# Performance work log

Hardware: AMD Instinct MI355X
Metric: run time of the kernel (lower is better)

## Reference

```python
import jax, jax.numpy as jnp
import numpy as np

MAX_FREQ = 4
OMEGA = 0.5 * np.pi
PATCH = 64


def _unnorm(c, size):
    # align_corners=False convention of torch.grid_sample
    return ((c + 1.0) * size - 1.0) / 2.0


def _gather(im, yy, xx):
    # im [C,H,W], yy/xx [Ho,Wo] -> [C,Ho,Wo]
    return im[:, yy, xx]


def _gs_nearest(inp, grid):
    # inp [B,C,H,W], grid [B,Ho,Wo,2] (x,y); padding_mode='border'
    B, C, H, W = inp.shape
    x = jnp.clip(jnp.round(_unnorm(grid[..., 0], W)), 0, W - 1).astype(jnp.int32)
    y = jnp.clip(jnp.round(_unnorm(grid[..., 1], H)), 0, H - 1).astype(jnp.int32)
    return jax.vmap(_gather)(inp, y, x)  # [B,C,Ho,Wo]


def _gs_bilinear(inp, grid):
    B, C, H, W = inp.shape
    x = jnp.clip(_unnorm(grid[..., 0], W), 0.0, W - 1.0)
    y = jnp.clip(_unnorm(grid[..., 1], H), 0.0, H - 1.0)
    x0 = jnp.floor(x); y0 = jnp.floor(y)
    wx = (x - x0)[:, None]; wy = (y - y0)[:, None]  # [B,1,Ho,Wo]
    x0i = x0.astype(jnp.int32); y0i = y0.astype(jnp.int32)
    x1i = jnp.minimum(x0i + 1, W - 1); y1i = jnp.minimum(y0i + 1, H - 1)
    g = jax.vmap(_gather)
    v00 = g(inp, y0i, x0i); v01 = g(inp, y0i, x1i)
    v10 = g(inp, y1i, x0i); v11 = g(inp, y1i, x1i)
    return (v00 * (1 - wx) * (1 - wy) + v01 * wx * (1 - wy)
            + v10 * (1 - wx) * wy + v11 * wx * wy)


def _conv2d(x, w, b):
    y = jax.lax.conv_general_dilated(x, w, (1, 1), ((1, 1), (1, 1)),
                                     dimension_numbers=("NCHW", "OIHW", "NCHW"))
    return y + b[None, :, None, None]


def _lc_decoder(q, rel):
    # q [B,Ho,Wo,2F+1], rel [B,Ho,Wo,1]; Fourier basis [1, cos(k*w*rel), sin(k*w*rel)]
    k = jnp.arange(1, MAX_FREQ + 1, dtype=q.dtype)
    ang = rel * k * OMEGA  # [B,Ho,Wo,F]
    basis = jnp.concatenate([jnp.ones_like(rel), jnp.cos(ang), jnp.sin(ang)], axis=-1)
    return jnp.sum(q * basis, axis=-1, keepdims=True)  # [B,Ho,Wo,1]


def _forward(sinogram, feat, grid, square_inv, adapt_w, adapt_b):
    B = feat.shape[0]
    sino = _conv2d(feat, adapt_w, adapt_b)          # [B,2F+1,V,D]
    V, D = sino.shape[-2], sino.shape[-1]
    # make_coord along detector axis (dim=1 coord channel), padding=0
    coord_d = ((jnp.arange(D, dtype=sino.dtype) + 0.5) / D) * 2.0 - 1.0
    sino_coord = jnp.broadcast_to(coord_d[None, None, None, :], (B, 1, V, D))
    shift_interval = 1.0 / D
    eps = 1e-4
    q_recons, lengths = [], []
    for sx in (-shift_interval, shift_interval):  # ensembling shifts
        g = grid + jnp.array([sx, 0.0], dtype=grid.dtype) + 1e-6
        q_recon = jnp.transpose(_gs_nearest(sino, g), (0, 2, 3, 1))       # [B,V,P2,2F+1]
        q_coord = jnp.transpose(_gs_nearest(sino_coord, g), (0, 2, 3, 1))  # [B,V,P2,1]
        rel = (grid[..., 0:1] - q_coord) * D
        q_recons.append(_lc_decoder(q_recon, rel))
        lengths.append(jnp.abs(rel) + eps)
    tot = lengths[0] + lengths[1]
    # lengths are swapped before weighting (cross weighting)
    recon = q_recons[0] * lengths[1] / tot + q_recons[1] * lengths[0] / tot
    out = jnp.sum(jnp.transpose(recon, (0, 3, 1, 2)) * square_inv * 10000.0, axis=-2)
    # back projection of center channel of raw sinogram
    ch = sinogram.shape[1]
    bp = _gs_bilinear(sinogram[:, ch // 2:ch // 2 + 1], grid)
    out = out + jnp.sum(bp * square_inv * 10000.0, axis=-2)  # [B,1,P2]
    return out.reshape(B, 1, PATCH, PATCH)


def setup_inputs() -> dict:
    key = jax.random.key(0)
    ks = jax.random.split(key, 6)
    B, V, D, ENC = 4, 360, 512, 64
    P2 = PATCH * PATCH
    CH = 2 * MAX_FREQ + 1
    return {
        "sinogram": jax.random.normal(ks[0], (B, 1, V, D), jnp.float32),
        "feat": jax.random.normal(ks[1], (B, ENC, V, D), jnp.float32),
        "grid": jax.random.uniform(ks[2], (B, V, P2, 2), jnp.float32, -1.0, 1.0),
        "square_inv": jax.random.uniform(ks[3], (B, 1, V, P2), jnp.float32, 1e-5, 1e-4),
        "adapt_w": jax.random.normal(ks[4], (CH, ENC, 3, 3), jnp.float32) * 0.05,
        "adapt_b": jax.random.normal(ks[5], (CH,), jnp.float32) * 0.05,
    }


def reference(sinogram, feat, grid, square_inv, adapt_w, adapt_b):
    return _forward(sinogram, feat, grid, square_inv, adapt_w, adapt_b)
```

## Files before the change

### kernel.cpp

```cpp
#include <hip/hip_runtime.h>
#include <hip/hip_fp16.h>
#include <math.h>

#define B   4
#define V   360
#define D   512
#define ENC 64
#define CH  9
#define P2  4096
#define NCHUNK 90
#define VCHUNK 4
#define DPT 4
#define RECH 16

__global__ __launch_bounds__(256) void conv_kernel(
    const float* __restrict__ feat,
    const float* __restrict__ w,
    const float* __restrict__ bias,
    __half* __restrict__ sino)
{
    const int bid = blockIdx.x;
    const int sw  = (bid & 7) * 90 + (bid >> 3);
    const int b   = sw / 180;
    const int vt  = sw % 180;
    const int tr  = threadIdx.x >> 7;
    const int v   = vt * 2 + tr;
    const int d0  = (threadIdx.x & 127) * DPT;

    float acc[CH][DPT];
    #pragma unroll
    for (int oc = 0; oc < CH; ++oc) {
        const float bv = bias[oc];
        #pragma unroll
        for (int p = 0; p < DPT; ++p) acc[oc][p] = bv;
    }

    const float* fb = feat + ((size_t)b * ENC * V + v) * D + d0;
    const bool vm = v > 0, vp = v < V - 1;
    const bool dm = d0 > 0, dp = (d0 + DPT) < D;

    for (int ic = 0; ic < ENC; ++ic) {
        const float* f = fb + (size_t)ic * (V * D);
        float r[3][DPT + 2];
        #pragma unroll
        for (int rr = 0; rr < 3; ++rr) {
            const float* fr = f + (rr - 1) * D;
            const bool ok = (rr == 0) ? vm : ((rr == 2) ? vp : true);
            float4 c = ok ? *(const float4*)fr : float4{0.f, 0.f, 0.f, 0.f};
            r[rr][1] = c.x; r[rr][2] = c.y; r[rr][3] = c.z; r[rr][4] = c.w;
            r[rr][0] = (ok && dm) ? fr[-1]  : 0.f;
            r[rr][5] = (ok && dp) ? fr[DPT] : 0.f;
        }
        #pragma unroll
        for (int oc = 0; oc < CH; ++oc) {
            const float* ww = w + ((size_t)oc * ENC + ic) * 9;
            #pragma unroll
            for (int kr = 0; kr < 3; ++kr) {
                #pragma unroll
                for (int kc = 0; kc < 3; ++kc) {
                    const float wv = ww[kr * 3 + kc];
                    #pragma unroll
                    for (int p = 0; p < DPT; ++p)
                        acc[oc][p] = fmaf(r[kr][p + kc], wv, acc[oc][p]);
                }
            }
        }
    }

    #pragma unroll
    for (int p = 0; p < DPT; ++p) {
        __half* rec = sino + (size_t)(((size_t)b * V + v) * D + d0 + p) * RECH;
        union { __half2 h; unsigned u; } cv;
        uint4 pk;
        cv.h = __floats2half2_rn(acc[0][p], acc[1][p]); pk.x = cv.u;
        cv.h = __floats2half2_rn(acc[2][p], acc[3][p]); pk.y = cv.u;
        cv.h = __floats2half2_rn(acc[4][p], acc[5][p]); pk.z = cv.u;
        cv.h = __floats2half2_rn(acc[6][p], acc[7][p]); pk.w = cv.u;
        *(uint4*)rec = pk;
        cv.h = __floats2half2_rn(acc[8][p], 0.f);
        *(unsigned*)(rec + 8) = cv.u;
    }
}

__global__ __launch_bounds__(256) void build_sg2(
    const float* __restrict__ sg, float2* __restrict__ sg2)
{
    const int i = blockIdx.x * 256 + threadIdx.x;
    const int x = i & (D - 1);
    const float a = sg[i];
    const float c = (x == D - 1) ? a : sg[i + 1];
    sg2[i] = float2{a, c};
}

template <int PAIRED>
__global__ __launch_bounds__(256) void sample_kernel(
    const __half* __restrict__ sino,
    const float* __restrict__ sinogram,
    const float2* __restrict__ sg2,
    const float* __restrict__ grid,
    const float* __restrict__ sq,
    float* __restrict__ partial)
{
    const int bid = blockIdx.x;
    const int xcd = bid & 7;
    const int b   = xcd >> 1;
    const int idx = ((bid >> 3) << 1) | (xcd & 1);
    const int chunk = idx >> 4;
    const int p  = (idx & 15) * 256 + threadIdx.x;
    const int v0 = chunk * VCHUNK;

    const float*  sg  = sinogram + (size_t)b * V * D;
    const float2* sg2b = sg2 + (size_t)b * V * D;
    const __half* sb  = sino + (size_t)b * V * D * RECH;

    float gx[4], gy[4], sv[4];
    #pragma unroll
    for (int u = 0; u < 4; ++u) {
        const size_t gi = (size_t)(b * V + v0 + u) * P2 + p;
        const double gd = __builtin_nontemporal_load((const double*)grid + gi);
        const unsigned long long gu = __double_as_longlong(gd);
        gx[u] = __uint_as_float((unsigned)gu);
        gy[u] = __uint_as_float((unsigned)(gu >> 32));
        sv[u] = __builtin_nontemporal_load(sq + gi);
    }

    uint4    ra[4][2];
    unsigned rzu[4][2];
    float    rel[4][2];
    #pragma unroll
    for (int u = 0; u < 4; ++u) {
        const float fy = ((gy[u] + 1e-6f + 1.f) * (float)V - 1.f) * 0.5f;
        const int   yi = (int)fminf(fmaxf(rintf(fy), 0.f), (float)(V - 1));
        const float fx0 = ((gx[u] + 1e-6f + 1.f) * (float)D - 1.f) * 0.5f;
        #pragma unroll
        for (int sft = 0; sft < 2; ++sft) {
            const float fx = (sft == 0) ? (fx0 - 0.5f) : (fx0 + 0.5f);
            const int   xi = (int)fminf(fmaxf(rintf(fx), 0.f), (float)(D - 1));
            const float qc = ((float)xi + 0.5f) * (2.f / (float)D) - 1.f;
            rel[u][sft] = (gx[u] - qc) * (float)D;
            const __half* rec = sb + (size_t)(yi * D + xi) * RECH;
            ra[u][sft]  = *(const uint4*)rec;
            rzu[u][sft] = *(const unsigned*)(rec + 8);
        }
    }

    float bl00[4], bl01[4], bl10[4], bl11[4], wxv[4], wyv[4];
    #pragma unroll
    for (int u = 0; u < 4; ++u) {
        float fxb = fminf(fmaxf(((gx[u] + 1.f) * (float)D - 1.f) * 0.5f, 0.f), (float)(D - 1));
        float fyb = fminf(fmaxf(((gy[u] + 1.f) * (float)V - 1.f) * 0.5f, 0.f), (float)(V - 1));
        const float x0 = floorf(fxb), y0 = floorf(fyb);
        wxv[u] = fxb - x0; wyv[u] = fyb - y0;
        const int x0i = (int)x0, y0i = (int)y0;
        const int y1i = min(y0i + 1, V - 1);
        if (PAIRED) {
            const float2 t = sg2b[y0i * D + x0i];
            const float2 u2 = sg2b[y1i * D + x0i];
            bl00[u] = t.x;  bl01[u] = t.y;
            bl10[u] = u2.x; bl11[u] = u2.y;
        } else {
            const int x1i = min(x0i + 1, D - 1);
            bl00[u] = sg[y0i * D + x0i]; bl01[u] = sg[y0i * D + x1i];
            bl10[u] = sg[y1i * D + x0i]; bl11[u] = sg[y1i * D + x1i];
        }
    }

    float acc = 0.f;
    #pragma unroll
    for (int u = 0; u < 4; ++u) {
        float val[2], len[2];
        #pragma unroll
        for (int sft = 0; sft < 2; ++sft) {
            float q[9];
            {
                const uint4 a = ra[u][sft];
                union { unsigned uu; __half2 h; } c;
                float2 f;
                c.uu = a.x; f = __half22float2(c.h); q[0] = f.x; q[1] = f.y;
                c.uu = a.y; f = __half22float2(c.h); q[2] = f.x; q[3] = f.y;
                c.uu = a.z; f = __half22float2(c.h); q[4] = f.x; q[5] = f.y;
                c.uu = a.w; f = __half22float2(c.h); q[6] = f.x; q[7] = f.y;
                union { unsigned short us; __half hh; } c2;
                c2.us = (unsigned short)rzu[u][sft];
                q[8] = __half2float(c2.hh);
            }
            const float r = rel[u][sft];
            const float ang = r * 1.5707963267948966f;
            float s1, c1;
            __sincosf(ang, &s1, &c1);
            const float c2 = fmaf(2.f * c1, c1, -1.f);
            const float s2 = 2.f * c1 * s1;
            const float c3 = fmaf(2.f * c1, c2, -c1);
            const float s3 = fmaf(2.f * c1, s2, -s1);
            const float c4 = fmaf(2.f * c1, c3, -c2);
            const float s4 = fmaf(2.f * c1, s3, -s2);

            float vv = q[0];
            vv = fmaf(q[1], c1, vv); vv = fmaf(q[2], c2, vv);
            vv = fmaf(q[3], c3, vv); vv = fmaf(q[4], c4, vv);
            vv = fmaf(q[5], s1, vv); vv = fmaf(q[6], s2, vv);
            vv = fmaf(q[7], s3, vv); vv = fmaf(q[8], s4, vv);
            val[sft] = vv;
            len[sft] = fabsf(r) + 1e-4f;
        }
        const float tot   = len[0] + len[1];
        const float recon = (val[0] * len[1] + val[1] * len[0]) / tot;

        const float wx = wxv[u], wy = wyv[u];
        const float bp = bl00[u] * (1.f - wx) * (1.f - wy) + bl01[u] * wx * (1.f - wy)
                       + bl10[u] * (1.f - wx) * wy         + bl11[u] * wx * wy;

        acc += (recon + bp) * sv[u] * 1e4f;
    }
    __builtin_nontemporal_store(acc, partial + ((size_t)chunk * B + b) * P2 + p);
}

__global__ __launch_bounds__(256) void reduce_kernel(
    const float* __restrict__ partial, float* __restrict__ out)
{
    const int i = blockIdx.x * 256 + threadIdx.x;
    float a = 0.f;
    #pragma unroll 6
    for (int c = 0; c < NCHUNK; ++c)
        a += __builtin_nontemporal_load(partial + (size_t)c * B * P2 + i);
    out[i] = a;
}

extern "C" void kernel_launch(void* const* d_in, const int* in_sizes, int n_in,
                              void* d_out, int out_size, void* d_ws, size_t ws_size,
                              hipStream_t stream)
{
    const float* sinogram = (const float*)d_in[0];
    const float* feat     = (const float*)d_in[1];
    const float* grid     = (const float*)d_in[2];
    const float* sq       = (const float*)d_in[3];
    const float* w        = (const float*)d_in[4];
    const float* bias     = (const float*)d_in[5];
    float* out = (float*)d_out;

    const size_t sino_b = (size_t)B * V * D * RECH * sizeof(__half);
    const size_t part_b = (size_t)NCHUNK * B * P2 * sizeof(float);
    const size_t sg2_b  = (size_t)B * V * D * sizeof(float2);

    __half* sino    = (__half*)d_ws;
    float*  partial = (float*)((char*)d_ws + sino_b);
    float2* sg2     = (float2*)((char*)d_ws + sino_b + part_b);
    const bool paired = (ws_size >= sino_b + part_b + sg2_b);

    conv_kernel<<<dim3(720), 256, 0, stream>>>(feat, w, bias, sino);
    if (paired) {
        build_sg2<<<dim3(2880), 256, 0, stream>>>(sinogram, sg2);
        sample_kernel<1><<<dim3(5760), 256, 0, stream>>>(sino, sinogram, sg2, grid, sq, partial);
    } else {
        sample_kernel<0><<<dim3(5760), 256, 0, stream>>>(sino, sinogram, sg2, grid, sq, partial);
    }
    reduce_kernel<<<dim3((B * P2) / 256), 256, 0, stream>>>(partial, out);
}
```

Baseline: 278.3 us.

## Store conv records as adjacent-pair entries so each sample does one fetch

The conv output is rewritten into a padded per-row layout of 513 64-byte entries. Each entry holds the records for detector columns x-1 and x side by side, so the two nearest-neighbour records a sample point needs sit in the same cache line. The conv kernel now computes two outputs per thread over 1440 blocks, double-buffers its input rows across channels, and writes each record twice. The aim is fewer scattered cache-line misses in the sampling gather, paid for with a larger intermediate buffer and more write traffic from the conv.

```diff
diff --git a/kernel.cpp b/kernel.cpp
--- a/kernel.cpp
+++ b/kernel.cpp
@@ -10,47 +10,49 @@
 #define P2  4096
 #define NCHUNK 90
 #define VCHUNK 4
-#define DPT 4
 #define RECH 16
-
+#define PENT 513
+#define PENTB 64
+
+template <int PAIR>
 __global__ __launch_bounds__(256) void conv_kernel(
     const float* __restrict__ feat,
     const float* __restrict__ w,
     const float* __restrict__ bias,
-    __half* __restrict__ sino)
+    char* __restrict__ outp)
 {
     const int bid = blockIdx.x;
-    const int sw  = (bid & 7) * 90 + (bid >> 3);
-    const int b   = sw / 180;
-    const int vt  = sw % 180;
-    const int tr  = threadIdx.x >> 7;
-    const int v   = vt * 2 + tr;
-    const int d0  = (threadIdx.x & 127) * DPT;
-
-    float acc[CH][DPT];
+    const int sw  = (bid & 7) * 180 + (bid >> 3);
+    const int b   = sw / V;
+    const int v   = sw % V;
+    const int d0  = threadIdx.x * 2;
+
+    float acc[CH][2];
     #pragma unroll
     for (int oc = 0; oc < CH; ++oc) {
         const float bv = bias[oc];
-        #pragma unroll
-        for (int p = 0; p < DPT; ++p) acc[oc][p] = bv;
+        acc[oc][0] = bv; acc[oc][1] = bv;
     }
 
     const float* fb = feat + ((size_t)b * ENC * V + v) * D + d0;
     const bool vm = v > 0, vp = v < V - 1;
-    const bool dm = d0 > 0, dp = (d0 + DPT) < D;
-
-    for (int ic = 0; ic < ENC; ++ic) {
+    const bool dm = d0 > 0, dp = d0 + 2 < D;
+
+    float r0[3][4], r1[3][4];
+
+    auto ld = [&](float r[3][4], int ic) {
         const float* f = fb + (size_t)ic * (V * D);
-        float r[3][DPT + 2];
         #pragma unroll
         for (int rr = 0; rr < 3; ++rr) {
             const float* fr = f + (rr - 1) * D;
             const bool ok = (rr == 0) ? vm : ((rr == 2) ? vp : true);
-            float4 c = ok ? *(const float4*)fr : float4{0.f, 0.f, 0.f, 0.f};
-            r[rr][1] = c.x; r[rr][2] = c.y; r[rr][3] = c.z; r[rr][4] = c.w;
-            r[rr][0] = (ok && dm) ? fr[-1]  : 0.f;
-            r[rr][5] = (ok && dp) ? fr[DPT] : 0.f;
-        }
+            float2 c = ok ? *(const float2*)fr : float2{0.f, 0.f};
+            r[rr][1] = c.x; r[rr][2] = c.y;
+            r[rr][0] = (ok && dm) ? fr[-1] : 0.f;
+            r[rr][3] = (ok && dp) ? fr[2]  : 0.f;
+        }
+    };
+    auto fmab = [&](const float r[3][4], int ic) {
         #pragma unroll
         for (int oc = 0; oc < CH; ++oc) {
             const float* ww = w + ((size_t)oc * ENC + ic) * 9;
@@ -59,26 +61,55 @@
                 #pragma unroll
                 for (int kc = 0; kc < 3; ++kc) {
                     const float wv = ww[kr * 3 + kc];
-                    #pragma unroll
-                    for (int p = 0; p < DPT; ++p)
-                        acc[oc][p] = fmaf(r[kr][p + kc], wv, acc[oc][p]);
+                    acc[oc][0] = fmaf(r[kr][kc],     wv, acc[oc][0]);
+                    acc[oc][1] = fmaf(r[kr][kc + 1], wv, acc[oc][1]);
                 }
             }
         }
-    }
-
-    #pragma unroll
-    for (int p = 0; p < DPT; ++p) {
-        __half* rec = sino + (size_t)(((size_t)b * V + v) * D + d0 + p) * RECH;
+    };
+
+    ld(r0, 0);
+    #pragma unroll 1
+    for (int ic = 0; ic < ENC; ic += 2) {
+        ld(r1, ic + 1);
+        fmab(r0, ic);
+        if (ic + 2 < ENC) ld(r0, ic + 2);
+        fmab(r1, ic + 1);
+    }
+
+    #pragma unroll
+    for (int p = 0; p < 2; ++p) {
         union { __half2 h; unsigned u; } cv;
         uint4 pk;
         cv.h = __floats2half2_rn(acc[0][p], acc[1][p]); pk.x = cv.u;
         cv.h = __floats2half2_rn(acc[2][p], acc[3][p]); pk.y = cv.u;
         cv.h = __floats2half2_rn(acc[4][p], acc[5][p]); pk.z = cv.u;
         cv.h = __floats2half2_rn(acc[6][p], acc[7][p]); pk.w = cv.u;
-        *(uint4*)rec = pk;
         cv.h = __floats2half2_rn(acc[8][p], 0.f);
-        *(unsigned*)(rec + 8) = cv.u;
+        const unsigned short z = (unsigned short)(cv.u & 0xffffu);
+        const int x = d0 + p;
+        if (PAIR) {
+            char* row = outp + (size_t)(b * V + v) * PENT * PENTB;
+            char* eA = row + (size_t)(x + 1) * PENTB;
+            *(uint4*)eA = pk;
+            *(unsigned short*)(eA + 32) = z;
+            char* eB = row + (size_t)x * PENTB + 16;
+            *(uint4*)eB = pk;
+            *(unsigned short*)(eB + 18) = z;
+            if (x == 0) {
+                *(uint4*)row = pk;
+                *(unsigned short*)(row + 32) = z;
+            }
+            if (x == D - 1) {
+                char* eC = row + (size_t)512 * PENTB + 16;
+                *(uint4*)eC = pk;
+                *(unsigned short*)(eC + 18) = z;
+            }
+        } else {
+            __half* rec = (__half*)outp + (size_t)(((size_t)b * V + v) * D + x) * RECH;
+            *(uint4*)rec = pk;
+            *(unsigned*)(rec + 8) = (unsigned)z;
+        }
     }
 }
 
@@ -92,10 +123,39 @@
     sg2[i] = float2{a, c};
 }
 
-template <int PAIRED>
-__global__ __launch_bounds__(256) void sample_kernel(
-    const __half* __restrict__ sino,
-    const float* __restrict__ sinogram,
+__device__ __forceinline__ float decode_rec(uint4 a, unsigned short z, float rel)
+{
+    float q[9];
+    union { unsigned uu; __half2 h; } c;
+    float2 f;
+    c.uu = a.x; f = __half22float2(c.h); q[0] = f.x; q[1] = f.y;
+    c.uu = a.y; f = __half22float2(c.h); q[2] = f.x; q[3] = f.y;
+    c.uu = a.z; f = __half22float2(c.h); q[4] = f.x; q[5] = f.y;
+    c.uu = a.w; f = __half22float2(c.h); q[6] = f.x; q[7] = f.y;
+    union { unsigned short us; __half hh; } c2;
+    c2.us = z;
+    q[8] = __half2float(c2.hh);
+
+    const float ang = rel * 1.5707963267948966f;
+    float s1, c1;
+    __sincosf(ang, &s1, &c1);
+    const float c2f = fmaf(2.f * c1, c1, -1.f);
+    const float s2f = 2.f * c1 * s1;
+    const float c3f = fmaf(2.f * c1, c2f, -c1);
+    const float s3f = fmaf(2.f * c1, s2f, -s1);
+    const float c4f = fmaf(2.f * c1, c3f, -c2f);
+    const float s4f = fmaf(2.f * c1, s3f, -s2f);
+
+    float vv = q[0];
+    vv = fmaf(q[1], c1,  vv); vv = fmaf(q[2], c2f, vv);
+    vv = fmaf(q[3], c3f, vv); vv = fmaf(q[4], c4f, vv);
+    vv = fmaf(q[5], s1,  vv); vv = fmaf(q[6], s2f, vv);
+    vv = fmaf(q[7], s3f, vv); vv = fmaf(q[8], s4f, vv);
+    return vv;
+}
+
+__global__ __launch_bounds__(256) void sample_pair(
+    const char* __restrict__ pair,
     const float2* __restrict__ sg2,
     const float* __restrict__ grid,
     const float* __restrict__ sq,
@@ -109,9 +169,8 @@
     const int p  = (idx & 15) * 256 + threadIdx.x;
     const int v0 = chunk * VCHUNK;
 
-    const float*  sg  = sinogram + (size_t)b * V * D;
-    const float2* sg2b = sg2 + (size_t)b * V * D;
-    const __half* sb  = sino + (size_t)b * V * D * RECH;
+    const char*   pb  = pair + (size_t)b * V * PENT * PENTB;
+    const float2* s2b = sg2 + (size_t)b * V * D;
 
     float gx[4], gy[4], sv[4];
     #pragma unroll
@@ -124,8 +183,96 @@
         sv[u] = __builtin_nontemporal_load(sq + gi);
     }
 
+    uint4 qa[4], qb[4];
+    unsigned short zA[4], zB[4];
+    float relm[4], relp[4];
+    #pragma unroll
+    for (int u = 0; u < 4; ++u) {
+        const float fy = ((gy[u] + 1e-6f + 1.f) * (float)V - 1.f) * 0.5f;
+        const int   yi = (int)fminf(fmaxf(rintf(fy), 0.f), (float)(V - 1));
+        const float fx0 = ((gx[u] + 1e-6f + 1.f) * (float)D - 1.f) * 0.5f;
+        const int xm = (int)fminf(fmaxf(rintf(fx0 - 0.5f), 0.f), (float)(D - 1));
+        const int xp = (int)fminf(fmaxf(rintf(fx0 + 0.5f), 0.f), (float)(D - 1));
+        const float qcm = ((float)xm + 0.5f) * (2.f / (float)D) - 1.f;
+        const float qcp = ((float)xp + 0.5f) * (2.f / (float)D) - 1.f;
+        relm[u] = (gx[u] - qcm) * (float)D;
+        relp[u] = (gx[u] - qcp) * (float)D;
+        const char* rowp = pb + (size_t)yi * (PENT * PENTB);
+        const char* e1 = rowp + (size_t)(xm + 1) * PENTB;
+        const char* e2 = rowp + (size_t)xp * PENTB;
+        qa[u] = *(const uint4*)e1;
+        zA[u] = *(const unsigned short*)(e1 + 32);
+        qb[u] = *(const uint4*)(e2 + 16);
+        zB[u] = *(const unsigned short*)(e2 + 34);
+    }
+
+    float bl00[4], bl01[4], bl10[4], bl11[4], wxv[4], wyv[4];
+    #pragma unroll
+    for (int u = 0; u < 4; ++u) {
+        float fxb = fminf(fmaxf(((gx[u] + 1.f) * (float)D - 1.f) * 0.5f, 0.f), (float)(D - 1));
+        float fyb = fminf(fmaxf(((gy[u] + 1.f) * (float)V - 1.f) * 0.5f, 0.f), (float)(V - 1));
+        const float x0 = floorf(fxb), y0 = floorf(fyb);
+        wxv[u] = fxb - x0; wyv[u] = fyb - y0;
+        const int x0i = (int)x0, y0i = (int)y0;
+        const int y1i = min(y0i + 1, V - 1);
+        const float2 t  = s2b[y0i * D + x0i];
+        const float2 u2 = s2b[y1i * D + x0i];
+        bl00[u] = t.x;  bl01[u] = t.y;
+        bl10[u] = u2.x; bl11[u] = u2.y;
+    }
+
+    float acc = 0.f;
+    #pragma unroll
+    for (int u = 0; u < 4; ++u) {
+        const float vmv = decode_rec(qa[u], zA[u], relm[u]);
+        const float vpv = decode_rec(qb[u], zB[u], relp[u]);
+        const float lm = fabsf(relm[u]) + 1e-4f;
+        const float lp = fabsf(relp[u]) + 1e-4f;
+        const float recon = (vmv * lp + vpv * lm) / (lm + lp);
+
+        const float wx = wxv[u], wy = wyv[u];
+        const float bp = bl00[u] * (1.f - wx) * (1.f - wy) + bl01[u] * wx * (1.f - wy)
+                       + bl10[u] * (1.f - wx) * wy         + bl11[u] * wx * wy;
+
+        acc += (recon + bp) * sv[u] * 1e4f;
+    }
+    __builtin_nontemporal_store(acc, partial + ((size_t)chunk * B + b) * P2 + p);
+}
+
+template <int PAIRED>
+__global__ __launch_bounds__(256) void sample_basic(
+    const __half* __restrict__ sino,
+    const float* __restrict__ sinogram,
+    const float2* __restrict__ sg2,
+    const float* __restrict__ grid,
+    const float* __restrict__ sq,
+    float* __restrict__ partial)
+{
+    const int bid = blockIdx.x;
+    const int xcd = bid & 7;
+    const int b   = xcd >> 1;
+    const int idx = ((bid >> 3) << 1) | (xcd & 1);
+    const int chunk = idx >> 4;
+    const int p  = (idx & 15) * 256 + threadIdx.x;
+    const int v0 = chunk * VCHUNK;
+
+    const float*  sg   = sinogram + (size_t)b * V * D;
+    const float2* s2b  = sg2 + (size_t)b * V * D;
+    const __half* sb   = sino + (size_t)b * V * D * RECH;
+
+    float gx[4], gy[4], sv[4];
+    #pragma unroll
+    for (int u = 0; u < 4; ++u) {
+        const size_t gi = (size_t)(b * V + v0 + u) * P2 + p;
+        const double gd = __builtin_nontemporal_load((const double*)grid + gi);
+        const unsigned long long gu = __double_as_longlong(gd);
+        gx[u] = __uint_as_float((unsigned)gu);
+        gy[u] = __uint_as_float((unsigned)(gu >> 32));
+        sv[u] = __builtin_nontemporal_load(sq + gi);
+    }
+
     uint4    ra[4][2];
-    unsigned rzu[4][2];
+    unsigned rz[4][2];
     float    rel[4][2];
     #pragma unroll
     for (int u = 0; u < 4; ++u) {
@@ -139,8 +286,8 @@
             const float qc = ((float)xi + 0.5f) * (2.f / (float)D) - 1.f;
             rel[u][sft] = (gx[u] - qc) * (float)D;
             const __half* rec = sb + (size_t)(yi * D + xi) * RECH;
-            ra[u][sft]  = *(const uint4*)rec;
-            rzu[u][sft] = *(const unsigned*)(rec + 8);
+            ra[u][sft] = *(const uint4*)rec;
+            rz[u][sft] = *(const unsigned*)(rec + 8);
         }
     }
 
@@ -154,8 +301,8 @@
         const int x0i = (int)x0, y0i = (int)y0;
         const int y1i = min(y0i + 1, V - 1);
         if (PAIRED) {
-            const float2 t = sg2b[y0i * D + x0i];
-            const float2 u2 = sg2b[y1i * D + x0i];
+            const float2 t  = s2b[y0i * D + x0i];
+            const float2 u2 = s2b[y1i * D + x0i];
             bl00[u] = t.x;  bl01[u] = t.y;
             bl10[u] = u2.x; bl11[u] = u2.y;
         } else {
@@ -168,48 +315,14 @@
     float acc = 0.f;
     #pragma unroll
     for (int u = 0; u < 4; ++u) {
-        float val[2], len[2];
-        #pragma unroll
-        for (int sft = 0; sft < 2; ++sft) {
-            float q[9];
-            {
-                const uint4 a = ra[u][sft];
-                union { unsigned uu; __half2 h; } c;
-                float2 f;
-                c.uu = a.x; f = __half22float2(c.h); q[0] = f.x; q[1] = f.y;
-                c.uu = a.y; f = __half22float2(c.h); q[2] = f.x; q[3] = f.y;
-                c.uu = a.z; f = __half22float2(c.h); q[4] = f.x; q[5] = f.y;
-                c.uu = a.w; f = __half22float2(c.h); q[6] = f.x; q[7] = f.y;
-                union { unsigned short us; __half hh; } c2;
-                c2.us = (unsigned short)rzu[u][sft];
-                q[8] = __half2float(c2.hh);
-            }
-            const float r = rel[u][sft];
-            const float ang = r * 1.5707963267948966f;
-            float s1, c1;
-            __sincosf(ang, &s1, &c1);
-            const float c2 = fmaf(2.f * c1, c1, -1.f);
-            const float s2 = 2.f * c1 * s1;
-            const float c3 = fmaf(2.f * c1, c2, -c1);
-            const float s3 = fmaf(2.f * c1, s2, -s1);
-            const float c4 = fmaf(2.f * c1, c3, -c2);
-            const float s4 = fmaf(2.f * c1, s3, -s2);
-
-            float vv = q[0];
-            vv = fmaf(q[1], c1, vv); vv = fmaf(q[2], c2, vv);
-            vv = fmaf(q[3], c3, vv); vv = fmaf(q[4], c4, vv);
-            vv = fmaf(q[5], s1, vv); vv = fmaf(q[6], s2, vv);
-            vv = fmaf(q[7], s3, vv); vv = fmaf(q[8], s4, vv);
-            val[sft] = vv;
-            len[sft] = fabsf(r) + 1e-4f;
-        }
-        const float tot   = len[0] + len[1];
-        const float recon = (val[0] * len[1] + val[1] * len[0]) / tot;
-
+        const float v0f = decode_rec(ra[u][0], (unsigned short)(rz[u][0] & 0xffffu), rel[u][0]);
+        const float v1f = decode_rec(ra[u][1], (unsigned short)(rz[u][1] & 0xffffu), rel[u][1]);
+        const float l0 = fabsf(rel[u][0]) + 1e-4f;
+        const float l1 = fabsf(rel[u][1]) + 1e-4f;
+        const float recon = (v0f * l1 + v1f * l0) / (l0 + l1);
         const float wx = wxv[u], wy = wyv[u];
         const float bp = bl00[u] * (1.f - wx) * (1.f - wy) + bl01[u] * wx * (1.f - wy)
                        + bl10[u] * (1.f - wx) * wy         + bl11[u] * wx * wy;
-
         acc += (recon + bp) * sv[u] * 1e4f;
     }
     __builtin_nontemporal_store(acc, partial + ((size_t)chunk * B + b) * P2 + p);
@@ -238,21 +351,32 @@
     const float* bias     = (const float*)d_in[5];
     float* out = (float*)d_out;
 
-    const size_t sino_b = (size_t)B * V * D * RECH * sizeof(__half);
+    const size_t pair_b = (size_t)B * V * PENT * PENTB;
     const size_t part_b = (size_t)NCHUNK * B * P2 * sizeof(float);
     const size_t sg2_b  = (size_t)B * V * D * sizeof(float2);
-
-    __half* sino    = (__half*)d_ws;
-    float*  partial = (float*)((char*)d_ws + sino_b);
-    float2* sg2     = (float2*)((char*)d_ws + sino_b + part_b);
-    const bool paired = (ws_size >= sino_b + part_b + sg2_b);
-
-    conv_kernel<<<dim3(720), 256, 0, stream>>>(feat, w, bias, sino);
-    if (paired) {
+    const size_t rec_b  = (size_t)B * V * D * RECH * sizeof(__half);
+
+    if (ws_size >= pair_b + part_b + sg2_b) {
+        char*   pair    = (char*)d_ws;
+        float*  partial = (float*)((char*)d_ws + pair_b);
+        float2* sg2     = (float2*)((char*)d_ws + pair_b + part_b);
+        conv_kernel<1><<<dim3(1440), 256, 0, stream>>>(feat, w, bias, pair);
         build_sg2<<<dim3(2880), 256, 0, stream>>>(sinogram, sg2);
-        sample_kernel<1><<<dim3(5760), 256, 0, stream>>>(sino, sinogram, sg2, grid, sq, partial);
+        sample_pair<<<dim3(5760), 256, 0, stream>>>(pair, sg2, grid, sq, partial);
+        reduce_kernel<<<dim3((B * P2) / 256), 256, 0, stream>>>(partial, out);
+    } else if (ws_size >= rec_b + part_b + sg2_b) {
+        char*   sino    = (char*)d_ws;
+        float*  partial = (float*)((char*)d_ws + rec_b);
+        float2* sg2     = (float2*)((char*)d_ws + rec_b + part_b);
+        conv_kernel<0><<<dim3(1440), 256, 0, stream>>>(feat, w, bias, sino);
+        build_sg2<<<dim3(2880), 256, 0, stream>>>(sinogram, sg2);
+        sample_basic<1><<<dim3(5760), 256, 0, stream>>>((const __half*)sino, sinogram, sg2, grid, sq, partial);
+        reduce_kernel<<<dim3((B * P2) / 256), 256, 0, stream>>>(partial, out);
     } else {
-        sample_kernel<0><<<dim3(5760), 256, 0, stream>>>(sino, sinogram, sg2, grid, sq, partial);
-    }
-    reduce_kernel<<<dim3((B * P2) / 256), 256, 0, stream>>>(partial, out);
-}
+        char*   sino    = (char*)d_ws;
+        float*  partial = (float*)((char*)d_ws + rec_b);
+        conv_kernel<0><<<dim3(1440), 256, 0, stream>>>(feat, w, bias, sino);
+        sample_basic<0><<<dim3(5760), 256, 0, stream>>>((const __half*)sino, sinogram, (const float2*)sino, grid, sq, partial);
+        reduce_kernel<<<dim3((B * P2) / 256), 256, 0, stream>>>(partial, out);
+    }
+}
```

After: 315.0 us. 1.13x slower.
